# Kernel optimization log

Measured on AMD Instinct MI355X. Metric: run time of the kernel, lower is better.

Reference implementation:

```python
import jax, jax.numpy as jnp
import numpy as np

EPS = 1e-5

def _ternary_ste(w):
    # STEQuantize: round(w/scale) clamped to [-1,1]; straight-through gradient.
    scale = jnp.maximum(jnp.mean(jnp.abs(w)), EPS)
    q = jnp.clip(jnp.round(w / scale), -1.0, 1.0)
    return w + jax.lax.stop_gradient(q - w)

def _bitlinear(x, w):
    # BitLinear: y = x @ (ternary(w) * scale)^T, scale = mean|w| (differentiable).
    scale = jnp.maximum(jnp.mean(jnp.abs(w)), EPS)
    return x @ (_ternary_ste(w) * scale).T

def _op_library(x, indices, weights, ops):
    # ops: (n_ops, D, D). Per-op ternary quantize + scale, then one batched einsum
    # instead of the python loop of small matmuls.
    n_ops = ops.shape[0]
    scales = jnp.maximum(jnp.mean(jnp.abs(ops), axis=(1, 2)), EPS)  # (n_ops,)
    q = jnp.clip(jnp.round(ops / scales[:, None, None]), -1.0, 1.0)
    w_eff = (ops + jax.lax.stop_gradient(q - ops)) * scales[:, None, None]  # (n,o,d)
    # transformed[n] = x @ w_eff[n]^T  ->  (B, S, n_ops, D)
    T = jnp.einsum('bsd,nod->bsno', x, w_eff)
    out = (1e-5 / n_ops) * jnp.sum(T, axis=2)
    gathered = jnp.take_along_axis(T, indices[:, :, :, None], axis=2)  # (B,S,K,D)
    out = out + jnp.sum(weights[..., None] * gathered, axis=2)
    return out

def _mem_read(x, slots, W_read):
    d = slots.shape[1]
    key = x @ W_read.T
    attn = jax.nn.softmax(key @ slots.T / jnp.sqrt(jnp.float32(d)), axis=-1)
    return attn @ slots

def _layernorm(x, gamma, beta):
    mu = jnp.mean(x, axis=-1, keepdims=True)
    var = jnp.var(x, axis=-1, keepdims=True)
    return (x - mu) * jax.lax.rsqrt(var + EPS) * gamma + beta

def _single_pass(reason, ops, W_router, slots, W_read, W_mix, ln_gamma, ln_beta, top_k):
    logits = _bitlinear(reason, W_router)              # (B,S,n_ops)
    vals, indices = jax.lax.top_k(logits, top_k)       # (B,S,K)
    weights = jax.nn.softmax(vals, axis=-1)
    op_out = _op_library(reason, indices, weights, ops)
    mem_out = _mem_read(reason, slots, W_read)
    mixed = jnp.concatenate([op_out, mem_out], axis=-1) @ W_mix.T
    return _layernorm(reason + mixed, ln_gamma, ln_beta)

def _write_signal(q, slots, W_wk, W_wg, W_wv):
    d = slots.shape[1]
    wk = q @ W_wk.T
    wg = jax.nn.sigmoid(q @ W_wg.T)                    # (B,S,1)
    wv = q @ W_wv.T
    addr = jax.nn.softmax(wk @ slots.T / jnp.sqrt(jnp.float32(d)), axis=-1)
    return wg * wv + 0.1 * (addr @ slots)

def setup_inputs() -> dict:
    key = jax.random.key(0)
    ks = jax.random.split(key, 12)
    B, S, d_model, d_reason = 8, 2048, 1024, 128
    n_ops, n_slots = 32, 16
    return {
        'hidden': jax.random.normal(ks[0], (B, S, d_model), jnp.float32),
        'force_depth': 2,
        'W_down': jax.random.normal(ks[1], (d_reason, d_model), jnp.float32) * 0.02,
        'W_up': jax.random.normal(ks[2], (d_model, d_reason), jnp.float32) * 0.02,
        'ops': jax.random.normal(ks[3], (n_ops, d_reason, d_reason), jnp.float32) * 0.02,
        'W_router': jax.random.normal(ks[4], (n_ops, d_reason), jnp.float32) * 0.02,
        'slots': jax.random.normal(ks[5], (n_slots, d_reason), jnp.float32) * 0.01,
        'W_read': jax.random.normal(ks[6], (d_reason, d_reason), jnp.float32) * 0.02,
        'W_wk': jax.random.normal(ks[7], (d_reason, d_reason), jnp.float32) * 0.02,
        'W_wg': jax.random.normal(ks[8], (1, d_reason), jnp.float32) * 0.02,
        'W_wv': jax.random.normal(ks[9], (d_reason, d_reason), jnp.float32) * 0.02,
        'W_mix': jax.random.normal(ks[10], (d_reason, 2 * d_reason), jnp.float32) * 0.02,
        'ln_gamma': jnp.ones((d_reason,), jnp.float32),
        'ln_beta': jnp.zeros((d_reason,), jnp.float32),
        'write_scale': jnp.float32(0.01),
    }

def reference(hidden, force_depth, W_down, W_up, ops, W_router, slots, W_read,
              W_wk, W_wg, W_wv, W_mix, ln_gamma, ln_beta, write_scale):
    top_k = 2
    reason = _bitlinear(hidden, W_down)
    for _ in range(int(force_depth)):
        reason = _single_pass(reason, ops, W_router, slots, W_read, W_mix,
                              ln_gamma, ln_beta, top_k)
    reason = reason + write_scale * _write_signal(reason, slots, W_wk, W_wg, W_wv)
    out = _bitlinear(reason, W_up)
    return hidden + out
```

## Files before the change

### kernel.cpp

```cpp
#include <hip/hip_runtime.h>


#define DR   128
#define DM   1024
#define NTOK 16384
#define NOPS 32
#define COEF (1e-5f / 32.f)

typedef __attribute__((ext_vector_type(8))) short bfrag;
typedef __attribute__((ext_vector_type(4))) float f32x4;

__device__ __forceinline__ ushort f2b_bits(float f) {
  union { float f; uint i; } c; c.f = f;
  uint x = c.i;
  return (ushort)((x + 0x7fffu + ((x >> 16) & 1u)) >> 16);
}
__device__ __forceinline__ float qeff(float w, float s) {
  float q = rintf(w / s);
  q = fminf(1.f, fmaxf(-1.f, q));
  return q * s;
}
__device__ __forceinline__ float waveRed(float v) {
#pragma unroll
  for (int m = 32; m > 0; m >>= 1) v += __shfl_xor(v, m, 64);
  return v;
}

#define OFF_SUMS    0
#define OFF_OPSSC   256
#define OFF_WDE     512
#define OFF_WUE     (OFF_WDE + 262144)
#define OFF_WRT     (OFF_WUE + 262144)
#define OFF_OPSB    (OFF_WRT + 16384)
#define OFF_WMIXA   (OFF_OPSB + 1048576)
#define OFF_WWVB    (OFF_WMIXA + 32768)
#define OFF_MRS     (OFF_WWVB + 32768)
#define OFF_MWS     (OFF_MRS + 8192)
#define OFF_SB      (OFF_MWS + 8192)
#define OFF_SLOTS   (OFF_SB + 8192)
#define OFF_WWG     (OFF_SLOTS + 8192)
#define OFF_GAMMA   (OFF_WWG + 512)
#define OFF_BETA    (OFF_GAMMA + 512)
#define OFF_WSC     (OFF_BETA + 512)
#define OFF_RF      (OFF_WSC + 256)
#define WS_TOTAL    (OFF_RF + 4194304)

__global__ __launch_bounds__(256) void k_absum(const float* __restrict__ w, int n,
                                               float* __restrict__ out) {
  __shared__ float ws4[4];
  float s = 0.f;
  for (int i = blockIdx.x * 256 + threadIdx.x; i < n; i += gridDim.x * 256)
    s += fabsf(w[i]);
  s = waveRed(s);
  int lane = threadIdx.x & 63, wv = threadIdx.x >> 6;
  if (lane == 0) ws4[wv] = s;
  __syncthreads();
  if (threadIdx.x == 0) atomicAdd(out, ws4[0] + ws4[1] + ws4[2] + ws4[3]);
}

__global__ __launch_bounds__(256) void k_absum_ops(const float* __restrict__ ops,
                                                   float* __restrict__ outs) {
  __shared__ float ws4[4];
  const int n = blockIdx.y;
  const float* w = ops + (size_t)n * (DR * DR);
  float s = 0.f;
  for (int i = blockIdx.x * 256 + threadIdx.x; i < DR * DR; i += gridDim.x * 256)
    s += fabsf(w[i]);
  s = waveRed(s);
  int lane = threadIdx.x & 63, wv = threadIdx.x >> 6;
  if (lane == 0) ws4[wv] = s;
  __syncthreads();
  if (threadIdx.x == 0) atomicAdd(&outs[n], ws4[0] + ws4[1] + ws4[2] + ws4[3]);
}

__global__ __launch_bounds__(256) void k_build(
    const float* __restrict__ W_down, const float* __restrict__ W_up,
    const float* __restrict__ W_router, const float* __restrict__ ops,
    const float* __restrict__ W_read, const float* __restrict__ W_wk,
    const float* __restrict__ W_wg, const float* __restrict__ W_wv,
    const float* __restrict__ W_mix, const float* __restrict__ slots,
    const float* __restrict__ gamma, const float* __restrict__ beta,
    const float* __restrict__ wscale, int has_wsc, const float* __restrict__ sums,
    ushort* __restrict__ WdE, ushort* __restrict__ WuE, float* __restrict__ WrT,
    ushort* __restrict__ opsB, float* __restrict__ opsScale,
    ushort* __restrict__ WmixA, ushort* __restrict__ WwvB,
    float* __restrict__ Mrs, float* __restrict__ Mws, float* __restrict__ SBw,
    float* __restrict__ slotsF, float* __restrict__ WwgF,
    float* __restrict__ gammaF, float* __restrict__ betaF, float* __restrict__ wscF) {
  int id = blockIdx.x * 256 + threadIdx.x;
  const float s_wd = fmaxf(sums[0] * (1.f / 131072.f), 1e-5f);
  const float s_wr = fmaxf(sums[1] * (1.f / 4096.f), 1e-5f);
  const float s_wu = fmaxf(sums[2] * (1.f / 131072.f), 1e-5f);

  if (id < 131072) { WdE[id] = f2b_bits(qeff(W_down[id], s_wd)); return; }
  id -= 131072;
  if (id < 131072) { WuE[id] = f2b_bits(qeff(W_up[id], s_wu)); return; }
  id -= 131072;
  if (id < 4096) {
    int d = id >> 5, n = id & 31;
    WrT[id] = qeff(W_router[n * DR + d], s_wr);
    return;
  }
  id -= 4096;
  if (id < 524288) {
    int n = id >> 14;
    float s = fmaxf(sums[3 + n] * (1.f / 16384.f), 1e-5f);
    float q = rintf(ops[id] / s);
    q = fminf(1.f, fmaxf(-1.f, q));
    opsB[id] = f2b_bits(q);
    return;
  }
  id -= 524288;
  if (id < 32) { opsScale[id] = fmaxf(sums[3 + id] * (1.f / 16384.f), 1e-5f); return; }
  id -= 32;
  if (id < 16384) {
    int r = id >> 7, o = id & 127;
    WmixA[id] = f2b_bits(W_mix[r * 256 + o]);
    return;
  }
  id -= 16384;
  if (id < 16384) { WwvB[id] = f2b_bits(W_wv[id]); return; }
  id -= 16384;
  if (id < 2048) {
    int d = id >> 4, j = id & 15;
    float a = 0.f;
    for (int o = 0; o < DR; ++o) a += W_read[o * DR + d] * slots[j * DR + o];
    Mrs[id] = a;
    return;
  }
  id -= 2048;
  if (id < 2048) {
    int d = id >> 4, j = id & 15;
    float a = 0.f;
    for (int o = 0; o < DR; ++o) a += W_wk[o * DR + d] * slots[j * DR + o];
    Mws[id] = a;
    return;
  }
  id -= 2048;
  if (id < 2048) {
    int j = id >> 7, r = id & 127;
    float a = 0.f;
    for (int o = 0; o < DR; ++o) a += slots[j * DR + o] * W_mix[r * 256 + 128 + o];
    SBw[id] = a;
    return;
  }
  id -= 2048;
  if (id < 2048) { slotsF[id] = slots[id]; return; }
  id -= 2048;
  if (id < 128) { WwgF[id] = W_wg[id]; return; }
  id -= 128;
  if (id < 128) { gammaF[id] = gamma[id]; return; }
  id -= 128;
  if (id < 128) { betaF[id] = beta[id]; return; }
  id -= 128;
  if (id == 0) { wscF[0] = has_wsc ? wscale[0] : 0.01f; }
}

__global__ __launch_bounds__(256) void k_down(const float* __restrict__ hidden,
                                              const ushort* __restrict__ WdE,
                                              float* __restrict__ X) {
  const int w = threadIdx.x >> 6, lane = threadIdx.x & 63;
  const int quad = lane >> 4, mrow = lane & 15;
  const int m0 = blockIdx.x * 32 + (w & 1) * 16;
  const int c0 = (w >> 1) * 64;

  f32x4 acc[4];
#pragma unroll
  for (int i = 0; i < 4; ++i) acc[i] = (f32x4){0.f, 0.f, 0.f, 0.f};

  const float* Ap = hidden + (size_t)(m0 + mrow) * DM + quad * 8;
  for (int kt = 0; kt < 32; ++kt) {
    float4 a0 = *(const float4*)(Ap + kt * 32);
    float4 a1 = *(const float4*)(Ap + kt * 32 + 4);
    bfrag a;
    a[0] = (short)f2b_bits(a0.x); a[1] = (short)f2b_bits(a0.y);
    a[2] = (short)f2b_bits(a0.z); a[3] = (short)f2b_bits(a0.w);
    a[4] = (short)f2b_bits(a1.x); a[5] = (short)f2b_bits(a1.y);
    a[6] = (short)f2b_bits(a1.z); a[7] = (short)f2b_bits(a1.w);
#pragma unroll
    for (int nt = 0; nt < 4; ++nt) {
      bfrag b = *(const bfrag*)(WdE + (size_t)(c0 + nt * 16 + mrow) * DM + kt * 32 + quad * 8);
      acc[nt] = __builtin_amdgcn_mfma_f32_16x16x32_bf16(a, b, acc[nt], 0, 0, 0);
    }
  }
#pragma unroll
  for (int nt = 0; nt < 4; ++nt)
#pragma unroll
    for (int r = 0; r < 4; ++r)
      X[(size_t)(m0 + quad * 4 + r) * DR + c0 + nt * 16 + mrow] = acc[nt][r];
}

__global__ __launch_bounds__(512) void k_pass2(
    float* __restrict__ X,
    const float* __restrict__ WrT, const ushort* __restrict__ opsB,
    const float* __restrict__ opsScale, const ushort* __restrict__ WmixA,
    const float* __restrict__ Mrs, const float* __restrict__ SBw,
    const float* __restrict__ gammaF, const float* __restrict__ betaF) {
  __shared__ float  xsf[64][128];
  __shared__ ushort xsb[64][136];
  __shared__ float  lg[64][32];
  __shared__ float  coefT[32][64];
  __shared__ float  attn[64][16];
  __shared__ int    seli[64][2];
  __shared__ float  selw[64][2];

  const int tid = threadIdx.x;
  const int w = tid >> 6, lane = tid & 63;
  const int quad = lane >> 4, mrow = lane & 15;
  const int t0 = blockIdx.x * 64;

  for (int i = tid; i < 2048; i += 512) {
    float4 v = *(const float4*)(X + (size_t)t0 * DR + i * 4);
    int t = i >> 5, c = (i & 31) * 4;
    xsf[t][c] = v.x; xsf[t][c + 1] = v.y; xsf[t][c + 2] = v.z; xsf[t][c + 3] = v.w;
    xsb[t][c] = f2b_bits(v.x); xsb[t][c + 1] = f2b_bits(v.y);
    xsb[t][c + 2] = f2b_bits(v.z); xsb[t][c + 3] = f2b_bits(v.w);
  }
  __syncthreads();

  for (int p = tid; p < 2048; p += 512) {
    int t = p >> 5, n = p & 31;
    float a = 0.f;
    for (int d = 0; d < DR; ++d) a += xsf[t][d] * WrT[d * 32 + n];
    lg[t][n] = a;
  }
  for (int p = tid; p < 1024; p += 512) {
    int t = p >> 4, j = p & 15;
    float a = 0.f;
    for (int d = 0; d < DR; ++d) a += xsf[t][d] * Mrs[d * 16 + j];
    attn[t][j] = a * 0.088388347648318447f;
  }
  __syncthreads();

  if (tid < 64) {
    float v0 = -1e30f; int i0 = 0;
#pragma unroll
    for (int n = 0; n < 32; ++n) { float v = lg[tid][n]; if (v > v0) { v0 = v; i0 = n; } }
    float v1 = -1e30f; int i1 = 0;
#pragma unroll
    for (int n = 0; n < 32; ++n)
      if (n != i0) { float v = lg[tid][n]; if (v > v1) { v1 = v; i1 = n; } }
    float e = expf(v1 - v0);
    float w0 = 1.f / (1.f + e);
    seli[tid][0] = i0; seli[tid][1] = i1;
    selw[tid][0] = w0; selw[tid][1] = e * w0;
    float m = -1e30f;
#pragma unroll
    for (int j = 0; j < 16; ++j) m = fmaxf(m, attn[tid][j]);
    float s = 0.f;
#pragma unroll
    for (int j = 0; j < 16; ++j) { float ee = expf(attn[tid][j] - m); attn[tid][j] = ee; s += ee; }
    float inv = 1.f / s;
#pragma unroll
    for (int j = 0; j < 16; ++j) attn[tid][j] *= inv;
  }
  __syncthreads();

  for (int p = tid; p < 2048; p += 512) {
    int n = p >> 6, t = p & 63;
    float cf = COEF;
    if (n == seli[t][0]) cf += selw[t][0];
    if (n == seli[t][1]) cf += selw[t][1];
    coefT[n][t] = cf * opsScale[n];
  }
  __syncthreads();

  bfrag a[4][4];
#pragma unroll
  for (int m = 0; m < 4; ++m)
#pragma unroll
    for (int kt = 0; kt < 4; ++kt)
      a[m][kt] = *(const bfrag*)&xsb[m * 16 + mrow][kt * 32 + quad * 8];

  const ushort* Bp = opsB + (size_t)(w * 16 + mrow) * DR + quad * 8;
  bfrag bc[4], bn[4];
#pragma unroll
  for (int kt = 0; kt < 4; ++kt) bc[kt] = *(const bfrag*)(Bp + kt * 32);

  f32x4 out[4];
#pragma unroll
  for (int m = 0; m < 4; ++m) out[m] = (f32x4){0.f, 0.f, 0.f, 0.f};

  for (int n = 0; n < NOPS; ++n) {
    if (n + 1 < NOPS) {
      const ushort* Bn = Bp + (size_t)(n + 1) * (DR * DR);
#pragma unroll
      for (int kt = 0; kt < 4; ++kt) bn[kt] = *(const bfrag*)(Bn + kt * 32);
    }
    f32x4 tmp[4];
#pragma unroll
    for (int m = 0; m < 4; ++m) tmp[m] = (f32x4){0.f, 0.f, 0.f, 0.f};
#pragma unroll
    for (int kt = 0; kt < 4; ++kt)
#pragma unroll
      for (int m = 0; m < 4; ++m)
        tmp[m] = __builtin_amdgcn_mfma_f32_16x16x32_bf16(a[m][kt], bc[kt], tmp[m], 0, 0, 0);
#pragma unroll
    for (int m = 0; m < 4; ++m) {
      f32x4 cf = *(const f32x4*)&coefT[n][m * 16 + quad * 4];
      out[m] += cf * tmp[m];
    }
    if (n + 1 < NOPS) {
#pragma unroll
      for (int kt = 0; kt < 4; ++kt) bc[kt] = bn[kt];
    }
  }
  __syncthreads();

#pragma unroll
  for (int m = 0; m < 4; ++m)
#pragma unroll
    for (int r = 0; r < 4; ++r)
      xsb[m * 16 + quad * 4 + r][w * 16 + mrow] = f2b_bits(out[m][r]);
  __syncthreads();

  if (w < 4) {
    bfrag a2[4];
#pragma unroll
    for (int kt = 0; kt < 4; ++kt)
      a2[kt] = *(const bfrag*)&xsb[w * 16 + mrow][kt * 32 + quad * 8];

    f32x4 acc[8];
#pragma unroll
    for (int i = 0; i < 8; ++i) acc[i] = (f32x4){0.f, 0.f, 0.f, 0.f};
#pragma unroll
    for (int kt = 0; kt < 4; ++kt)
#pragma unroll
      for (int nt = 0; nt < 8; ++nt) {
        bfrag b = *(const bfrag*)(WmixA + (size_t)(nt * 16 + mrow) * DR + kt * 32 + quad * 8);
        acc[nt] = __builtin_amdgcn_mfma_f32_16x16x32_bf16(a2[kt], b, acc[nt], 0, 0, 0);
      }

    float v[8][4];
#pragma unroll
    for (int nt = 0; nt < 8; ++nt) {
      const int col = nt * 16 + mrow;
#pragma unroll
      for (int r = 0; r < 4; ++r) {
        const int t = w * 16 + quad * 4 + r;
        float y0 = 0.f;
#pragma unroll
        for (int j = 0; j < 16; ++j) y0 += attn[t][j] * SBw[j * 128 + col];
        v[nt][r] = acc[nt][r] + xsf[t][col] + y0;
      }
    }
    float s[4], q[4];
#pragma unroll
    for (int r = 0; r < 4; ++r) {
      float ps = 0.f, pq = 0.f;
#pragma unroll
      for (int nt = 0; nt < 8; ++nt) { ps += v[nt][r]; pq += v[nt][r] * v[nt][r]; }
      s[r] = ps; q[r] = pq;
    }
#pragma unroll
    for (int m = 1; m < 16; m <<= 1)
#pragma unroll
      for (int r = 0; r < 4; ++r) {
        s[r] += __shfl_xor(s[r], m, 64);
        q[r] += __shfl_xor(q[r], m, 64);
      }
    float mu[4], rsd[4];
#pragma unroll
    for (int r = 0; r < 4; ++r) {
      mu[r] = s[r] * (1.f / DR);
      float var = q[r] * (1.f / DR) - mu[r] * mu[r];
      rsd[r] = rsqrtf(var + 1e-5f);
    }
#pragma unroll
    for (int nt = 0; nt < 8; ++nt) {
      const int col = nt * 16 + mrow;
      const float g = gammaF[col], bb = betaF[col];
#pragma unroll
      for (int r = 0; r < 4; ++r) {
        const int t = w * 16 + quad * 4 + r;
        X[(size_t)(t0 + t) * DR + col] = (v[nt][r] - mu[r]) * rsd[r] * g + bb;
      }
    }
  }
}

__global__ __launch_bounds__(256) void k_wsig(
    const float* __restrict__ X, ushort* __restrict__ RF,
    const ushort* __restrict__ WwvB, const float* __restrict__ Mws,
    const float* __restrict__ slotsF, const float* __restrict__ WwgF,
    const float* __restrict__ wscF) {
  __shared__ float  xsf[64][128];
  __shared__ ushort xsb[64][136];
  __shared__ float  attn[64][16];
  __shared__ float  gp[64];

  const int tid = threadIdx.x;
  const int w = tid >> 6, lane = tid & 63;
  const int quad = lane >> 4, mrow = lane & 15;
  const int t0 = blockIdx.x * 64;
  const float wsc = wscF[0];

  for (int i = tid; i < 2048; i += 256) {
    float4 v = *(const float4*)(X + (size_t)t0 * DR + i * 4);
    int t = i >> 5, c = (i & 31) * 4;
    xsf[t][c] = v.x; xsf[t][c + 1] = v.y; xsf[t][c + 2] = v.z; xsf[t][c + 3] = v.w;
    xsb[t][c] = f2b_bits(v.x); xsb[t][c + 1] = f2b_bits(v.y);
    xsb[t][c + 2] = f2b_bits(v.z); xsb[t][c + 3] = f2b_bits(v.w);
  }
  __syncthreads();

  for (int p = tid; p < 1024; p += 256) {
    int t = p >> 4, j = p & 15;
    float a = 0.f;
    for (int d = 0; d < DR; ++d) a += xsf[t][d] * Mws[d * 16 + j];
    attn[t][j] = a * 0.088388347648318447f;
  }
  __syncthreads();

  if (tid < 64) {
    float z = 0.f;
    for (int d = 0; d < DR; ++d) z += xsf[tid][d] * WwgF[d];
    gp[tid] = wsc / (1.f + expf(-z));
    float m = -1e30f;
#pragma unroll
    for (int j = 0; j < 16; ++j) m = fmaxf(m, attn[tid][j]);
    float s = 0.f;
#pragma unroll
    for (int j = 0; j < 16; ++j) { float e = expf(attn[tid][j] - m); attn[tid][j] = e; s += e; }
    float inv = 1.f / s;
#pragma unroll
    for (int j = 0; j < 16; ++j) attn[tid][j] *= inv;
  }
  __syncthreads();

  bfrag a2[4];
#pragma unroll
  for (int kt = 0; kt < 4; ++kt)
    a2[kt] = *(const bfrag*)&xsb[w * 16 + mrow][kt * 32 + quad * 8];

  f32x4 acc[8];
#pragma unroll
  for (int i = 0; i < 8; ++i) acc[i] = (f32x4){0.f, 0.f, 0.f, 0.f};
#pragma unroll
  for (int kt = 0; kt < 4; ++kt)
#pragma unroll
    for (int nt = 0; nt < 8; ++nt) {
      bfrag b = *(const bfrag*)(WwvB + (size_t)(nt * 16 + mrow) * DR + kt * 32 + quad * 8);
      acc[nt] = __builtin_amdgcn_mfma_f32_16x16x32_bf16(a2[kt], b, acc[nt], 0, 0, 0);
    }

  const float c01 = wsc * 0.1f;
#pragma unroll
  for (int nt = 0; nt < 8; ++nt) {
    const int col = nt * 16 + mrow;
#pragma unroll
    for (int r = 0; r < 4; ++r) {
      const int t = w * 16 + quad * 4 + r;
      float mo = 0.f;
#pragma unroll
      for (int j = 0; j < 16; ++j) mo += attn[t][j] * slotsF[j * DR + col];
      float val = xsf[t][col] + gp[t] * acc[nt][r] + c01 * mo;
      RF[(size_t)(t0 + t) * DR + col] = f2b_bits(val);
    }
  }
}

__global__ __launch_bounds__(256) void k_up(const ushort* __restrict__ Rf,
                                            const ushort* __restrict__ WuE,
                                            const float* __restrict__ hidden,
                                            float* __restrict__ out) {
  const int wave = threadIdx.x >> 6, lane = threadIdx.x & 63;
  const int quad = lane >> 4, mrow = lane & 15;
  const int mt = blockIdx.x >> 3, ngrp = blockIdx.x & 7;
  const int m0 = mt * 64 + wave * 16;
  const int ng = ngrp * 8;

  f32x4 acc[8];
#pragma unroll
  for (int i = 0; i < 8; ++i) acc[i] = (f32x4){0.f, 0.f, 0.f, 0.f};

  const ushort* Ap = Rf + (size_t)(m0 + mrow) * DR + quad * 8;
#pragma unroll
  for (int kt = 0; kt < 4; ++kt) {
    bfrag a = *(const bfrag*)(Ap + kt * 32);
#pragma unroll
    for (int nt = 0; nt < 8; ++nt) {
      const ushort* Bp = WuE + (size_t)((ng + nt) * 16 + mrow) * DR + kt * 32 + quad * 8;
      bfrag b = *(const bfrag*)Bp;
      acc[nt] = __builtin_amdgcn_mfma_f32_16x16x32_bf16(a, b, acc[nt], 0, 0, 0);
    }
  }
#pragma unroll
  for (int nt = 0; nt < 8; ++nt)
#pragma unroll
    for (int r = 0; r < 4; ++r) {
      const int token = m0 + quad * 4 + r;
      const int j = (ng + nt) * 16 + mrow;
      const size_t idx = (size_t)token * DM + j;
      out[idx] = hidden[idx] + acc[nt][r];
    }
}

extern "C" void kernel_launch(void* const* d_in, const int* in_sizes, int n_in,
                              void* d_out, int out_size, void* d_ws, size_t ws_size,
                              hipStream_t stream) {
  int ns[20]; int nn = 0; int lastsc = -1;
  for (int i = 0; i < n_in; ++i) {
    if (in_sizes[i] == 1) lastsc = i;
    else if (nn < 20) ns[nn++] = i;
  }
  int iH = 0, iWd = 2, iWu = 3, iOps = 4, iWr = 5, iSl = 6, iRe = 7,
      iWk = 8, iWg = 9, iWv = 10, iMx = 11, iG = 12, iB = 13;
  if (nn >= 13) {
    iH  = ns[0];  iWd = ns[1];  iWu = ns[2];  iOps = ns[3]; iWr = ns[4];
    iSl = ns[5];  iRe = ns[6];  iWk = ns[7];  iWg = ns[8];  iWv = ns[9];
    iMx = ns[10]; iG  = ns[11]; iB  = ns[12];
  }
  const float* hidden   = (const float*)d_in[iH];
  const float* W_down   = (const float*)d_in[iWd];
  const float* W_up     = (const float*)d_in[iWu];
  const float* opsw     = (const float*)d_in[iOps];
  const float* W_router = (const float*)d_in[iWr];
  const float* slots    = (const float*)d_in[iSl];
  const float* W_read   = (const float*)d_in[iRe];
  const float* W_wk     = (const float*)d_in[iWk];
  const float* W_wg     = (const float*)d_in[iWg];
  const float* W_wv     = (const float*)d_in[iWv];
  const float* W_mix    = (const float*)d_in[iMx];
  const float* lng      = (const float*)d_in[iG];
  const float* lnb      = (const float*)d_in[iB];
  const float* wscale   = (lastsc >= 0) ? (const float*)d_in[lastsc] : (const float*)d_in[iG];
  const int has_wsc     = (lastsc >= 0) ? 1 : 0;

  char* ws = (char*)d_ws;
  float*  sums   = (float*)(ws + OFF_SUMS);
  float*  opsSc  = (float*)(ws + OFF_OPSSC);
  ushort* WdE    = (ushort*)(ws + OFF_WDE);
  ushort* WuE    = (ushort*)(ws + OFF_WUE);
  float*  WrT    = (float*)(ws + OFF_WRT);
  ushort* opsB   = (ushort*)(ws + OFF_OPSB);
  ushort* WmixA  = (ushort*)(ws + OFF_WMIXA);
  ushort* WwvB   = (ushort*)(ws + OFF_WWVB);
  float*  Mrs    = (float*)(ws + OFF_MRS);
  float*  Mws    = (float*)(ws + OFF_MWS);
  float*  SBw    = (float*)(ws + OFF_SB);
  float*  slotsF = (float*)(ws + OFF_SLOTS);
  float*  WwgF   = (float*)(ws + OFF_WWG);
  float*  gammaF = (float*)(ws + OFF_GAMMA);
  float*  betaF  = (float*)(ws + OFF_BETA);
  float*  wscF   = (float*)(ws + OFF_WSC);
  ushort* RF     = (ushort*)(ws + OFF_RF);

  float* X = (float*)d_out;

  hipMemsetAsync(ws + OFF_SUMS, 0, 256, stream);
  k_absum<<<128, 256, 0, stream>>>(W_down, 131072, &sums[0]);
  k_absum<<<4, 256, 0, stream>>>(W_router, 4096, &sums[1]);
  k_absum<<<128, 256, 0, stream>>>(W_up, 131072, &sums[2]);
  k_absum_ops<<<dim3(4, 32), 256, 0, stream>>>(opsw, sums + 3);
  k_build<<<3250, 256, 0, stream>>>(W_down, W_up, W_router, opsw, W_read, W_wk, W_wg,
                                    W_wv, W_mix, slots, lng, lnb, wscale, has_wsc,
                                    sums, WdE, WuE, WrT, opsB, opsSc, WmixA, WwvB,
                                    Mrs, Mws, SBw, slotsF, WwgF, gammaF, betaF, wscF);
  k_down<<<512, 256, 0, stream>>>(hidden, WdE, X);
  for (int pass = 0; pass < 2; ++pass)
    k_pass2<<<256, 512, 0, stream>>>(X, WrT, opsB, opsSc, WmixA, Mrs, SBw,
                                     gammaF, betaF);
  k_wsig<<<256, 256, 0, stream>>>(X, RF, WwvB, Mws, slotsF, WwgF, wscF);
  k_up<<<2048, 256, 0, stream>>>(RF, WuE, hidden, X);
}
```

Baseline: 397.6 us.

## Fuse absum launches and write-signal into pass, halve tiles, coalesce up-proj epilogue

Merges the four abs-sum reduction launches into one grid, fuses the write-signal computation into the second reasoning pass so the intermediate reason tensor is not written and re-read, and halves the token tile in k_pass2 and k_down to launch twice as many blocks. k_up now stages its accumulator tile in shared memory so the hidden-residual read and output write use coalesced float4 accesses. Smaller tiles improve occupancy and wave count but reload the op weights more often per token, and the fused pass adds shared memory and a longer tail to its last launch.

```diff
diff --git a/kernel.cpp b/kernel.cpp
--- a/kernel.cpp
+++ b/kernel.cpp
@@ -45,32 +45,25 @@
 #define OFF_RF      (OFF_WSC + 256)
 #define WS_TOTAL    (OFF_RF + 4194304)
 
-__global__ __launch_bounds__(256) void k_absum(const float* __restrict__ w, int n,
-                                               float* __restrict__ out) {
+__global__ __launch_bounds__(256) void k_absum_all(
+    const float* __restrict__ W_down, const float* __restrict__ W_router,
+    const float* __restrict__ W_up, const float* __restrict__ ops,
+    float* __restrict__ sums) {
   __shared__ float ws4[4];
+  const int y = blockIdx.y;
+  const float* src; int n; float* dst;
+  if (y == 0)      { src = W_down;   n = 131072; dst = &sums[0]; }
+  else if (y == 1) { src = W_router; n = 4096;   dst = &sums[1]; }
+  else if (y == 2) { src = W_up;     n = 131072; dst = &sums[2]; }
+  else { src = ops + (size_t)(y - 3) * 16384; n = 16384; dst = &sums[y]; }
   float s = 0.f;
-  for (int i = blockIdx.x * 256 + threadIdx.x; i < n; i += gridDim.x * 256)
-    s += fabsf(w[i]);
+  for (int i = blockIdx.x * 256 + threadIdx.x; i < n; i += 8 * 256)
+    s += fabsf(src[i]);
   s = waveRed(s);
   int lane = threadIdx.x & 63, wv = threadIdx.x >> 6;
   if (lane == 0) ws4[wv] = s;
   __syncthreads();
-  if (threadIdx.x == 0) atomicAdd(out, ws4[0] + ws4[1] + ws4[2] + ws4[3]);
-}
-
-__global__ __launch_bounds__(256) void k_absum_ops(const float* __restrict__ ops,
-                                                   float* __restrict__ outs) {
-  __shared__ float ws4[4];
-  const int n = blockIdx.y;
-  const float* w = ops + (size_t)n * (DR * DR);
-  float s = 0.f;
-  for (int i = blockIdx.x * 256 + threadIdx.x; i < DR * DR; i += gridDim.x * 256)
-    s += fabsf(w[i]);
-  s = waveRed(s);
-  int lane = threadIdx.x & 63, wv = threadIdx.x >> 6;
-  if (lane == 0) ws4[wv] = s;
-  __syncthreads();
-  if (threadIdx.x == 0) atomicAdd(&outs[n], ws4[0] + ws4[1] + ws4[2] + ws4[3]);
+  if (threadIdx.x == 0) atomicAdd(dst, ws4[0] + ws4[1] + ws4[2] + ws4[3]);
 }
 
 __global__ __launch_bounds__(256) void k_build(
@@ -161,14 +154,15 @@
                                               float* __restrict__ X) {
   const int w = threadIdx.x >> 6, lane = threadIdx.x & 63;
   const int quad = lane >> 4, mrow = lane & 15;
-  const int m0 = blockIdx.x * 32 + (w & 1) * 16;
-  const int c0 = (w >> 1) * 64;
-
-  f32x4 acc[4];
-#pragma unroll
-  for (int i = 0; i < 4; ++i) acc[i] = (f32x4){0.f, 0.f, 0.f, 0.f};
+  const int m0 = blockIdx.x * 16;
+  const int c0 = w * 32;
+
+  f32x4 acc[2];
+  acc[0] = (f32x4){0.f, 0.f, 0.f, 0.f};
+  acc[1] = (f32x4){0.f, 0.f, 0.f, 0.f};
 
   const float* Ap = hidden + (size_t)(m0 + mrow) * DM + quad * 8;
+#pragma unroll 2
   for (int kt = 0; kt < 32; ++kt) {
     float4 a0 = *(const float4*)(Ap + kt * 32);
     float4 a1 = *(const float4*)(Ap + kt * 32 + 4);
@@ -178,38 +172,43 @@
     a[4] = (short)f2b_bits(a1.x); a[5] = (short)f2b_bits(a1.y);
     a[6] = (short)f2b_bits(a1.z); a[7] = (short)f2b_bits(a1.w);
 #pragma unroll
-    for (int nt = 0; nt < 4; ++nt) {
+    for (int nt = 0; nt < 2; ++nt) {
       bfrag b = *(const bfrag*)(WdE + (size_t)(c0 + nt * 16 + mrow) * DM + kt * 32 + quad * 8);
       acc[nt] = __builtin_amdgcn_mfma_f32_16x16x32_bf16(a, b, acc[nt], 0, 0, 0);
     }
   }
 #pragma unroll
-  for (int nt = 0; nt < 4; ++nt)
+  for (int nt = 0; nt < 2; ++nt)
 #pragma unroll
     for (int r = 0; r < 4; ++r)
       X[(size_t)(m0 + quad * 4 + r) * DR + c0 + nt * 16 + mrow] = acc[nt][r];
 }
 
 __global__ __launch_bounds__(512) void k_pass2(
-    float* __restrict__ X,
+    float* __restrict__ X, ushort* __restrict__ RF, int emit,
     const float* __restrict__ WrT, const ushort* __restrict__ opsB,
     const float* __restrict__ opsScale, const ushort* __restrict__ WmixA,
     const float* __restrict__ Mrs, const float* __restrict__ SBw,
-    const float* __restrict__ gammaF, const float* __restrict__ betaF) {
-  __shared__ float  xsf[64][128];
-  __shared__ ushort xsb[64][136];
-  __shared__ float  lg[64][32];
-  __shared__ float  coefT[32][64];
-  __shared__ float  attn[64][16];
-  __shared__ int    seli[64][2];
-  __shared__ float  selw[64][2];
+    const float* __restrict__ gammaF, const float* __restrict__ betaF,
+    const ushort* __restrict__ WwvB, const float* __restrict__ Mws,
+    const float* __restrict__ slotsF, const float* __restrict__ WwgF,
+    const float* __restrict__ wscF) {
+  __shared__ float  xsf[32][128];
+  __shared__ ushort xsb[32][136];
+  __shared__ float  lg[32][32];
+  __shared__ float  coefT[32][32];
+  __shared__ float  attn[32][16];
+  __shared__ float  at2[32][16];
+  __shared__ int    seli[32][2];
+  __shared__ float  selw[32][2];
+  __shared__ float  gp[32];
 
   const int tid = threadIdx.x;
   const int w = tid >> 6, lane = tid & 63;
   const int quad = lane >> 4, mrow = lane & 15;
-  const int t0 = blockIdx.x * 64;
-
-  for (int i = tid; i < 2048; i += 512) {
+  const int t0 = blockIdx.x * 32;
+
+  for (int i = tid; i < 1024; i += 512) {
     float4 v = *(const float4*)(X + (size_t)t0 * DR + i * 4);
     int t = i >> 5, c = (i & 31) * 4;
     xsf[t][c] = v.x; xsf[t][c + 1] = v.y; xsf[t][c + 2] = v.z; xsf[t][c + 3] = v.w;
@@ -218,21 +217,25 @@
   }
   __syncthreads();
 
-  for (int p = tid; p < 2048; p += 512) {
+  for (int p = tid; p < 1024; p += 512) {
     int t = p >> 5, n = p & 31;
     float a = 0.f;
+#pragma unroll 8
     for (int d = 0; d < DR; ++d) a += xsf[t][d] * WrT[d * 32 + n];
     lg[t][n] = a;
   }
-  for (int p = tid; p < 1024; p += 512) {
-    int t = p >> 4, j = p & 15;
-    float a = 0.f;
-    for (int d = 0; d < DR; ++d) a += xsf[t][d] * Mrs[d * 16 + j];
-    attn[t][j] = a * 0.088388347648318447f;
-  }
-  __syncthreads();
-
-  if (tid < 64) {
+  {
+    int t = tid >> 4, j = tid & 15;
+    if (tid < 512) {
+      float a = 0.f;
+#pragma unroll 8
+      for (int d = 0; d < DR; ++d) a += xsf[t][d] * Mrs[d * 16 + j];
+      attn[t][j] = a * 0.088388347648318447f;
+    }
+  }
+  __syncthreads();
+
+  if (tid < 32) {
     float v0 = -1e30f; int i0 = 0;
 #pragma unroll
     for (int n = 0; n < 32; ++n) { float v = lg[tid][n]; if (v > v0) { v0 = v; i0 = n; } }
@@ -256,8 +259,8 @@
   }
   __syncthreads();
 
-  for (int p = tid; p < 2048; p += 512) {
-    int n = p >> 6, t = p & 63;
+  for (int p = tid; p < 1024; p += 512) {
+    int n = p >> 5, t = p & 31;
     float cf = COEF;
     if (n == seli[t][0]) cf += selw[t][0];
     if (n == seli[t][1]) cf += selw[t][1];
@@ -265,9 +268,9 @@
   }
   __syncthreads();
 
-  bfrag a[4][4];
-#pragma unroll
-  for (int m = 0; m < 4; ++m)
+  bfrag a[2][4];
+#pragma unroll
+  for (int m = 0; m < 2; ++m)
 #pragma unroll
     for (int kt = 0; kt < 4; ++kt)
       a[m][kt] = *(const bfrag*)&xsb[m * 16 + mrow][kt * 32 + quad * 8];
@@ -277,9 +280,9 @@
 #pragma unroll
   for (int kt = 0; kt < 4; ++kt) bc[kt] = *(const bfrag*)(Bp + kt * 32);
 
-  f32x4 out[4];
-#pragma unroll
-  for (int m = 0; m < 4; ++m) out[m] = (f32x4){0.f, 0.f, 0.f, 0.f};
+  f32x4 out[2];
+  out[0] = (f32x4){0.f, 0.f, 0.f, 0.f};
+  out[1] = (f32x4){0.f, 0.f, 0.f, 0.f};
 
   for (int n = 0; n < NOPS; ++n) {
     if (n + 1 < NOPS) {
@@ -287,16 +290,16 @@
 #pragma unroll
       for (int kt = 0; kt < 4; ++kt) bn[kt] = *(const bfrag*)(Bn + kt * 32);
     }
-    f32x4 tmp[4];
-#pragma unroll
-    for (int m = 0; m < 4; ++m) tmp[m] = (f32x4){0.f, 0.f, 0.f, 0.f};
+    f32x4 tmp[2];
+    tmp[0] = (f32x4){0.f, 0.f, 0.f, 0.f};
+    tmp[1] = (f32x4){0.f, 0.f, 0.f, 0.f};
 #pragma unroll
     for (int kt = 0; kt < 4; ++kt)
 #pragma unroll
-      for (int m = 0; m < 4; ++m)
+      for (int m = 0; m < 2; ++m)
         tmp[m] = __builtin_amdgcn_mfma_f32_16x16x32_bf16(a[m][kt], bc[kt], tmp[m], 0, 0, 0);
 #pragma unroll
-    for (int m = 0; m < 4; ++m) {
+    for (int m = 0; m < 2; ++m) {
       f32x4 cf = *(const f32x4*)&coefT[n][m * 16 + quad * 4];
       out[m] += cf * tmp[m];
     }
@@ -308,13 +311,13 @@
   __syncthreads();
 
 #pragma unroll
-  for (int m = 0; m < 4; ++m)
+  for (int m = 0; m < 2; ++m)
 #pragma unroll
     for (int r = 0; r < 4; ++r)
       xsb[m * 16 + quad * 4 + r][w * 16 + mrow] = f2b_bits(out[m][r]);
   __syncthreads();
 
-  if (w < 4) {
+  if (w < 2) {
     bfrag a2[4];
 #pragma unroll
     for (int kt = 0; kt < 4; ++kt)
@@ -366,96 +369,94 @@
       float var = q[r] * (1.f / DR) - mu[r] * mu[r];
       rsd[r] = rsqrtf(var + 1e-5f);
     }
-#pragma unroll
-    for (int nt = 0; nt < 8; ++nt) {
-      const int col = nt * 16 + mrow;
-      const float g = gammaF[col], bb = betaF[col];
+    if (!emit) {
+#pragma unroll
+      for (int nt = 0; nt < 8; ++nt) {
+        const int col = nt * 16 + mrow;
+        const float g = gammaF[col], bb = betaF[col];
+#pragma unroll
+        for (int r = 0; r < 4; ++r) {
+          const int t = w * 16 + quad * 4 + r;
+          X[(size_t)(t0 + t) * DR + col] = (v[nt][r] - mu[r]) * rsd[r] * g + bb;
+        }
+      }
+    } else {
+#pragma unroll
+      for (int nt = 0; nt < 8; ++nt) {
+        const int col = nt * 16 + mrow;
+        const float g = gammaF[col], bb = betaF[col];
+#pragma unroll
+        for (int r = 0; r < 4; ++r) {
+          const int t = w * 16 + quad * 4 + r;
+          float val = (v[nt][r] - mu[r]) * rsd[r] * g + bb;
+          xsf[t][col] = val;
+          xsb[t][col] = f2b_bits(val);
+        }
+      }
+    }
+  }
+  if (!emit) return;
+
+  __syncthreads();
+
+  {
+    int t = tid >> 4, j = tid & 15;
+    float a = 0.f;
+#pragma unroll 8
+    for (int d = 0; d < DR; ++d) a += xsf[t][d] * Mws[d * 16 + j];
+    at2[t][j] = a * 0.088388347648318447f;
+  }
+  __syncthreads();
+
+  if (tid < 32) {
+    float z = 0.f;
+#pragma unroll 8
+    for (int d = 0; d < DR; ++d) z += xsf[tid][d] * WwgF[d];
+    gp[tid] = wscF[0] / (1.f + expf(-z));
+    float m = -1e30f;
+#pragma unroll
+    for (int j = 0; j < 16; ++j) m = fmaxf(m, at2[tid][j]);
+    float s = 0.f;
+#pragma unroll
+    for (int j = 0; j < 16; ++j) { float e = expf(at2[tid][j] - m); at2[tid][j] = e; s += e; }
+    float inv = 1.f / s;
+#pragma unroll
+    for (int j = 0; j < 16; ++j) at2[tid][j] *= inv;
+  }
+  __syncthreads();
+
+  if (w < 4) {
+    const int mtile = w & 1;
+    const int ch = (w >> 1) * 64;
+    bfrag a2[4];
+#pragma unroll
+    for (int kt = 0; kt < 4; ++kt)
+      a2[kt] = *(const bfrag*)&xsb[mtile * 16 + mrow][kt * 32 + quad * 8];
+
+    f32x4 acc[4];
+#pragma unroll
+    for (int i = 0; i < 4; ++i) acc[i] = (f32x4){0.f, 0.f, 0.f, 0.f};
+#pragma unroll
+    for (int kt = 0; kt < 4; ++kt)
+#pragma unroll
+      for (int nt = 0; nt < 4; ++nt) {
+        bfrag b = *(const bfrag*)(WwvB + (size_t)(ch + nt * 16 + mrow) * DR + kt * 32 + quad * 8);
+        acc[nt] = __builtin_amdgcn_mfma_f32_16x16x32_bf16(a2[kt], b, acc[nt], 0, 0, 0);
+      }
+
+    const float c01 = wscF[0] * 0.1f;
+#pragma unroll
+    for (int nt = 0; nt < 4; ++nt) {
+      const int col = ch + nt * 16 + mrow;
 #pragma unroll
       for (int r = 0; r < 4; ++r) {
-        const int t = w * 16 + quad * 4 + r;
-        X[(size_t)(t0 + t) * DR + col] = (v[nt][r] - mu[r]) * rsd[r] * g + bb;
-      }
-    }
-  }
-}
-
-__global__ __launch_bounds__(256) void k_wsig(
-    const float* __restrict__ X, ushort* __restrict__ RF,
-    const ushort* __restrict__ WwvB, const float* __restrict__ Mws,
-    const float* __restrict__ slotsF, const float* __restrict__ WwgF,
-    const float* __restrict__ wscF) {
-  __shared__ float  xsf[64][128];
-  __shared__ ushort xsb[64][136];
-  __shared__ float  attn[64][16];
-  __shared__ float  gp[64];
-
-  const int tid = threadIdx.x;
-  const int w = tid >> 6, lane = tid & 63;
-  const int quad = lane >> 4, mrow = lane & 15;
-  const int t0 = blockIdx.x * 64;
-  const float wsc = wscF[0];
-
-  for (int i = tid; i < 2048; i += 256) {
-    float4 v = *(const float4*)(X + (size_t)t0 * DR + i * 4);
-    int t = i >> 5, c = (i & 31) * 4;
-    xsf[t][c] = v.x; xsf[t][c + 1] = v.y; xsf[t][c + 2] = v.z; xsf[t][c + 3] = v.w;
-    xsb[t][c] = f2b_bits(v.x); xsb[t][c + 1] = f2b_bits(v.y);
-    xsb[t][c + 2] = f2b_bits(v.z); xsb[t][c + 3] = f2b_bits(v.w);
-  }
-  __syncthreads();
-
-  for (int p = tid; p < 1024; p += 256) {
-    int t = p >> 4, j = p & 15;
-    float a = 0.f;
-    for (int d = 0; d < DR; ++d) a += xsf[t][d] * Mws[d * 16 + j];
-    attn[t][j] = a * 0.088388347648318447f;
-  }
-  __syncthreads();
-
-  if (tid < 64) {
-    float z = 0.f;
-    for (int d = 0; d < DR; ++d) z += xsf[tid][d] * WwgF[d];
-    gp[tid] = wsc / (1.f + expf(-z));
-    float m = -1e30f;
-#pragma unroll
-    for (int j = 0; j < 16; ++j) m = fmaxf(m, attn[tid][j]);
-    float s = 0.f;
-#pragma unroll
-    for (int j = 0; j < 16; ++j) { float e = expf(attn[tid][j] - m); attn[tid][j] = e; s += e; }
-    float inv = 1.f / s;
-#pragma unroll
-    for (int j = 0; j < 16; ++j) attn[tid][j] *= inv;
-  }
-  __syncthreads();
-
-  bfrag a2[4];
-#pragma unroll
-  for (int kt = 0; kt < 4; ++kt)
-    a2[kt] = *(const bfrag*)&xsb[w * 16 + mrow][kt * 32 + quad * 8];
-
-  f32x4 acc[8];
-#pragma unroll
-  for (int i = 0; i < 8; ++i) acc[i] = (f32x4){0.f, 0.f, 0.f, 0.f};
-#pragma unroll
-  for (int kt = 0; kt < 4; ++kt)
-#pragma unroll
-    for (int nt = 0; nt < 8; ++nt) {
-      bfrag b = *(const bfrag*)(WwvB + (size_t)(nt * 16 + mrow) * DR + kt * 32 + quad * 8);
-      acc[nt] = __builtin_amdgcn_mfma_f32_16x16x32_bf16(a2[kt], b, acc[nt], 0, 0, 0);
-    }
-
-  const float c01 = wsc * 0.1f;
-#pragma unroll
-  for (int nt = 0; nt < 8; ++nt) {
-    const int col = nt * 16 + mrow;
-#pragma unroll
-    for (int r = 0; r < 4; ++r) {
-      const int t = w * 16 + quad * 4 + r;
-      float mo = 0.f;
-#pragma unroll
-      for (int j = 0; j < 16; ++j) mo += attn[t][j] * slotsF[j * DR + col];
-      float val = xsf[t][col] + gp[t] * acc[nt][r] + c01 * mo;
-      RF[(size_t)(t0 + t) * DR + col] = f2b_bits(val);
+        const int t = mtile * 16 + quad * 4 + r;
+        float mo = 0.f;
+#pragma unroll
+        for (int j = 0; j < 16; ++j) mo += at2[t][j] * slotsF[j * DR + col];
+        float val = xsf[t][col] + gp[t] * acc[nt][r] + c01 * mo;
+        RF[(size_t)(t0 + t) * DR + col] = f2b_bits(val);
+      }
     }
   }
 }
@@ -464,11 +465,14 @@
                                             const ushort* __restrict__ WuE,
                                             const float* __restrict__ hidden,
                                             float* __restrict__ out) {
+  __shared__ float cs[64][132];
+
   const int wave = threadIdx.x >> 6, lane = threadIdx.x & 63;
   const int quad = lane >> 4, mrow = lane & 15;
   const int mt = blockIdx.x >> 3, ngrp = blockIdx.x & 7;
-  const int m0 = mt * 64 + wave * 16;
-  const int ng = ngrp * 8;
+  const int m0b = mt * 64;
+  const int m0 = m0b + wave * 16;
+  const int c0 = ngrp * 128;
 
   f32x4 acc[8];
 #pragma unroll
@@ -480,7 +484,7 @@
     bfrag a = *(const bfrag*)(Ap + kt * 32);
 #pragma unroll
     for (int nt = 0; nt < 8; ++nt) {
-      const ushort* Bp = WuE + (size_t)((ng + nt) * 16 + mrow) * DR + kt * 32 + quad * 8;
+      const ushort* Bp = WuE + (size_t)(c0 + nt * 16 + mrow) * DR + kt * 32 + quad * 8;
       bfrag b = *(const bfrag*)Bp;
       acc[nt] = __builtin_amdgcn_mfma_f32_16x16x32_bf16(a, b, acc[nt], 0, 0, 0);
     }
@@ -488,12 +492,23 @@
 #pragma unroll
   for (int nt = 0; nt < 8; ++nt)
 #pragma unroll
-    for (int r = 0; r < 4; ++r) {
-      const int token = m0 + quad * 4 + r;
-      const int j = (ng + nt) * 16 + mrow;
-      const size_t idx = (size_t)token * DM + j;
-      out[idx] = hidden[idx] + acc[nt][r];
-    }
+    for (int r = 0; r < 4; ++r)
+      cs[wave * 16 + quad * 4 + r][nt * 16 + mrow] = acc[nt][r];
+  __syncthreads();
+
+#pragma unroll
+  for (int k = 0; k < 8; ++k) {
+    const int i = threadIdx.x + k * 256;
+    const int t = i >> 5, c4 = (i & 31) * 4;
+    const size_t idx = (size_t)(m0b + t) * DM + c0 + c4;
+    float4 h = *(const float4*)(hidden + idx);
+    float4 v;
+    v.x = h.x + cs[t][c4];
+    v.y = h.y + cs[t][c4 + 1];
+    v.z = h.z + cs[t][c4 + 2];
+    v.w = h.w + cs[t][c4 + 3];
+    *(float4*)(out + idx) = v;
+  }
 }
 
 extern "C" void kernel_launch(void* const* d_in, const int* in_sizes, int n_in,
@@ -549,18 +564,15 @@
   float* X = (float*)d_out;
 
   hipMemsetAsync(ws + OFF_SUMS, 0, 256, stream);
-  k_absum<<<128, 256, 0, stream>>>(W_down, 131072, &sums[0]);
-  k_absum<<<4, 256, 0, stream>>>(W_router, 4096, &sums[1]);
-  k_absum<<<128, 256, 0, stream>>>(W_up, 131072, &sums[2]);
-  k_absum_ops<<<dim3(4, 32), 256, 0, stream>>>(opsw, sums + 3);
+  k_absum_all<<<dim3(8, 35), 256, 0, stream>>>(W_down, W_router, W_up, opsw, sums);
   k_build<<<3250, 256, 0, stream>>>(W_down, W_up, W_router, opsw, W_read, W_wk, W_wg,
                                     W_wv, W_mix, slots, lng, lnb, wscale, has_wsc,
                                     sums, WdE, WuE, WrT, opsB, opsSc, WmixA, WwvB,
                                     Mrs, Mws, SBw, slotsF, WwgF, gammaF, betaF, wscF);
-  k_down<<<512, 256, 0, stream>>>(hidden, WdE, X);
-  for (int pass = 0; pass < 2; ++pass)
-    k_pass2<<<256, 512, 0, stream>>>(X, WrT, opsB, opsSc, WmixA, Mrs, SBw,
-                                     gammaF, betaF);
-  k_wsig<<<256, 256, 0, stream>>>(X, RF, WwvB, Mws, slotsF, WwgF, wscF);
+  k_down<<<1024, 256, 0, stream>>>(hidden, WdE, X);
+  k_pass2<<<512, 512, 0, stream>>>(X, RF, 0, WrT, opsB, opsSc, WmixA, Mrs, SBw,
+                                   gammaF, betaF, WwvB, Mws, slotsF, WwgF, wscF);
+  k_pass2<<<512, 512, 0, stream>>>(X, RF, 1, WrT, opsB, opsSc, WmixA, Mrs, SBw,
+                                   gammaF, betaF, WwvB, Mws, slotsF, WwgF, wscF);
   k_up<<<2048, 256, 0, stream>>>(RF, WuE, hidden, X);
 }
```

Measured after the change: 457.4 us. +15.0%, slower.
